# Optimization experiments

Hardware: AMD Instinct MI355X
Metric: run time of the kernel (lower is better)

## Reference

```python
import jax, jax.numpy as jnp
import numpy as np

# Dimensions (see FeatureMixer.__init__ / forward)
B, Q, H, P, C_HEAD = 4, 900, 4, 32, 64          # C_HEAD = feats_dim // num_heads
FEATS_DIM, QUERY_DIM, E = 256, 256, 2
EP = E * P                                        # 64 expanded points
PARAM1 = FEATS_DIM * EP                           # 16384
PARAM2 = EP * P * H                               # 8192
TOTAL = PARAM1 + PARAM2                           # 24576
D1 = PARAM1 // (H * C_HEAD)                       # 64 hidden dim after channel mixing
OUT_IN = PARAM2 * E                               # 16384 = H*EP*D1, out_proj in_features
EPS = 1e-5


def _ln2d(x):
    # F.layer_norm over the last two dims, no affine
    m = jnp.mean(x, axis=(-2, -1), keepdims=True)
    v = jnp.mean((x - m) ** 2, axis=(-2, -1), keepdims=True)
    return (x - m) * jax.lax.rsqrt(v + EPS)


def setup_inputs() -> dict:
    key = jax.random.key(0)
    ks = jax.random.split(key, 6)
    return {
        "query_feats": jax.random.normal(ks[0], (B, Q, QUERY_DIM), jnp.float32),
        "sampled_features": jax.random.normal(ks[1], (B, Q, H, P, C_HEAD), jnp.float32),
        "W_gen": jax.random.normal(ks[2], (QUERY_DIM, TOTAL), jnp.float32) * 0.02,
        "b_gen": jax.random.normal(ks[3], (TOTAL,), jnp.float32) * 0.02,
        "W_out": jax.random.normal(ks[4], (OUT_IN, QUERY_DIM), jnp.float32) * 0.02,
        "b_out": jnp.zeros((QUERY_DIM,), jnp.float32),
        "ln_w": jnp.ones((QUERY_DIM,), jnp.float32),
        "ln_b": jnp.zeros((QUERY_DIM,), jnp.float32),
    }


def reference(query_feats, sampled_features, W_gen, b_gen, W_out, b_out, ln_w, ln_b):
    # generate per-query mixing parameters: (B,Q,TOTAL)
    params = query_feats @ W_gen + b_gen
    p1 = params[..., :PARAM1].reshape(B, Q, H, C_HEAD, D1)   # channel mixer
    p2 = params[..., PARAM1:].reshape(B, Q, H, EP, P)        # spatial mixer

    # channel mixing: (B,Q,H,P,C) @ (B,Q,H,C,D1) -> (B,Q,H,P,D1)
    out = jnp.einsum('bqhpc,bqhcd->bqhpd', sampled_features, p1)
    out = _ln2d(jax.nn.gelu(out, approximate=False))

    # spatial mixing: (B,Q,H,EP,P) @ (B,Q,H,P,D1) -> (B,Q,H,EP,D1)
    out = jnp.einsum('bqhep,bqhpd->bqhed', p2, out)
    out = _ln2d(jax.nn.gelu(out, approximate=False))

    # project back to query dim + affine LayerNorm
    out = out.reshape(B, Q, OUT_IN) @ W_out + b_out
    m = jnp.mean(out, axis=-1, keepdims=True)
    v = jnp.mean((out - m) ** 2, axis=-1, keepdims=True)
    return (out - m) * jax.lax.rsqrt(v + EPS) * ln_w + ln_b
```

## Files before the change

kernel.cpp:

```cpp
#include <hip/hip_runtime.h>
#include <hip/hip_bf16.h>


typedef __attribute__((ext_vector_type(8))) __bf16 bf16x8;
typedef __attribute__((ext_vector_type(4))) float f32x4;
typedef __attribute__((ext_vector_type(4))) short short4v;
typedef __attribute__((ext_vector_type(8))) short short8v;

#define BQ_TOT 3600

__device__ __forceinline__ short f2bf(float f) {
  __hip_bfloat16 h = __float2bfloat16(f);
  short s; __builtin_memcpy(&s, &h, 2);
  return s;
}
__device__ __forceinline__ bf16x8 pack8(float4 a, float4 b) {
  short8v o;
  o[0] = f2bf(a.x); o[1] = f2bf(a.y); o[2] = f2bf(a.z); o[3] = f2bf(a.w);
  o[4] = f2bf(b.x); o[5] = f2bf(b.y); o[6] = f2bf(b.z); o[7] = f2bf(b.w);
  return __builtin_bit_cast(bf16x8, o);
}
__device__ __forceinline__ float gelu_f(float x) {
  float x2 = x * x;
  float u = x * (0.7978845608f + 0.0356774081f * x2);
  float e = __builtin_amdgcn_exp2f(u * 2.885390082f);
  float t = 1.0f - 2.0f / (e + 1.0f);
  return 0.5f * x * (1.0f + t);
}
__device__ __forceinline__ void wred2(float& a, float& b) {
#pragma unroll
  for (int m = 32; m >= 1; m >>= 1) {
    a += __shfl_xor(a, m, 64);
    b += __shfl_xor(b, m, 64);
  }
}

__global__ __launch_bounds__(256) void kcvt_f2b(const float* __restrict__ in,
                                                short* __restrict__ out) {
  int idx = (blockIdx.x * 256 + threadIdx.x) * 8;
  const float4* p = (const float4*)(in + idx);
  *(short8v*)(void*)(out + idx) = __builtin_bit_cast(short8v, pack8(p[0], p[1]));
}

__global__ __launch_bounds__(256) void ktrans_f2b(const float* __restrict__ in,
                                                  short* __restrict__ out,
                                                  int R, int C) {
  __shared__ float t[32][33];
  int tx = threadIdx.x & 31, ty = threadIdx.x >> 5;
  int r0 = blockIdx.y * 32, c0 = blockIdx.x * 32;
#pragma unroll
  for (int i = 0; i < 4; i++)
    t[ty + i * 8][tx] = in[(size_t)(r0 + ty + i * 8) * C + c0 + tx];
  __syncthreads();
#pragma unroll
  for (int i = 0; i < 4; i++)
    out[(size_t)(c0 + ty + i * 8) * R + r0 + tx] = f2bf(t[tx][ty + i * 8]);
}

__global__ __launch_bounds__(256) void k1t_gemm(const short* __restrict__ Xb,
                                                const short* __restrict__ WT,
                                                const float* __restrict__ bg,
                                                short* __restrict__ par,
                                                int nrows) {
  __shared__ short smem[128 * 40 * 2];
  short* As = smem;
  short* Bs = smem + 128 * 40;
  const int b = blockIdx.x;
  const int xcd = b & 7, i = b >> 3;
  const int ct = xcd * 24 + i / 29;
  const int rt = i % 29;
  const int tid = threadIdx.x;
  const int lane = tid & 63, wv = tid >> 6;
  const int l15 = lane & 15, quad = lane >> 4;
  const int wm = (wv & 1) * 64, wn = (wv >> 1) * 64;
  const int sm = tid >> 1, sk = (tid & 1) * 16;
  f32x4 acc[4][4] = {};
  for (int k0 = 0; k0 < 256; k0 += 32) {
    uint4 a0 = {0, 0, 0, 0}, a1 = {0, 0, 0, 0};
    int gr = rt * 128 + sm;
    if (gr < nrows) {
      const uint4* pa = (const uint4*)(Xb + (size_t)gr * 256 + k0 + sk);
      a0 = pa[0]; a1 = pa[1];
    }
    *(uint4*)(As + sm * 40 + sk) = a0;
    *(uint4*)(As + sm * 40 + sk + 8) = a1;
    const uint4* pb = (const uint4*)(WT + (size_t)(ct * 128 + sm) * 256 + k0 + sk);
    *(uint4*)(Bs + sm * 40 + sk) = pb[0];
    *(uint4*)(Bs + sm * 40 + sk + 8) = pb[1];
    __syncthreads();
    bf16x8 af[4], bfr[4];
#pragma unroll
    for (int i2 = 0; i2 < 4; i2++)
      af[i2] = *(const bf16x8*)(const void*)(As + (wm + i2 * 16 + l15) * 40 + quad * 8);
#pragma unroll
    for (int j = 0; j < 4; j++)
      bfr[j] = *(const bf16x8*)(const void*)(Bs + (wn + j * 16 + l15) * 40 + quad * 8);
#pragma unroll
    for (int i2 = 0; i2 < 4; i2++)
#pragma unroll
      for (int j = 0; j < 4; j++)
        acc[i2][j] = __builtin_amdgcn_mfma_f32_16x16x32_bf16(af[i2], bfr[j], acc[i2][j], 0, 0, 0);
    __syncthreads();
  }
  short* Cs = smem;
#pragma unroll
  for (int h = 0; h < 2; h++) {
    if ((wv & 1) == h) {
#pragma unroll
      for (int i2 = 0; i2 < 4; i2++)
#pragma unroll
        for (int j = 0; j < 4; j++) {
          float bgv = bg[ct * 128 + wn + j * 16 + l15];
#pragma unroll
          for (int r = 0; r < 4; r++)
            Cs[(i2 * 16 + quad * 4 + r) * 136 + wn + j * 16 + l15] =
                f2bf(acc[i2][j][r] + bgv);
        }
    }
    __syncthreads();
#pragma unroll
    for (int it = 0; it < 4; it++) {
      int rr = it * 16 + (tid >> 4);
      int cc = (tid & 15) * 8;
      uint4 v = *(const uint4*)(const void*)(Cs + rr * 136 + cc);
      int row = rt * 128 + h * 64 + rr;
      if (row < nrows)
        *(uint4*)(par + (size_t)row * 24576 + ct * 128 + cc) = v;
    }
    __syncthreads();
  }
}

__global__ __launch_bounds__(256) void k1_gemm(const float* __restrict__ X,
                                               const float* __restrict__ Wg,
                                               const float* __restrict__ bg,
                                               short* __restrict__ par,
                                               int nrows) {
  __shared__ short As[128 * 40];
  __shared__ short Bs[128 * 40];
  const int tid = threadIdx.x;
  const int rt = blockIdx.x, ct = blockIdx.y;
  const int lane = tid & 63, wv = tid >> 6;
  const int l15 = lane & 15, quad = lane >> 4;
  const int wm = (wv & 1) * 64, wn = (wv >> 1) * 64;
  const int sm = tid >> 1, sk = (tid & 1) * 16;
  const int bk = tid >> 3, bn0 = (tid & 7) * 16;
  f32x4 acc[4][4] = {};
  for (int k0 = 0; k0 < 256; k0 += 32) {
    float4 av[4] = {};
    int gr = rt * 128 + sm;
    if (gr < nrows) {
      const float4* pa = (const float4*)(X + (size_t)gr * 256 + k0 + sk);
      av[0] = pa[0]; av[1] = pa[1]; av[2] = pa[2]; av[3] = pa[3];
    }
    *(short8v*)(void*)(As + sm * 40 + sk) = __builtin_bit_cast(short8v, pack8(av[0], av[1]));
    *(short8v*)(void*)(As + sm * 40 + sk + 8) = __builtin_bit_cast(short8v, pack8(av[2], av[3]));
    const float4* pb = (const float4*)(Wg + (size_t)(k0 + bk) * 24576 + ct * 128 + bn0);
    float4 b0 = pb[0], b1 = pb[1], b2 = pb[2], b3 = pb[3];
    short* bd = Bs + bn0 * 40 + bk;
    bd[0 * 40] = f2bf(b0.x); bd[1 * 40] = f2bf(b0.y); bd[2 * 40] = f2bf(b0.z); bd[3 * 40] = f2bf(b0.w);
    bd[4 * 40] = f2bf(b1.x); bd[5 * 40] = f2bf(b1.y); bd[6 * 40] = f2bf(b1.z); bd[7 * 40] = f2bf(b1.w);
    bd[8 * 40] = f2bf(b2.x); bd[9 * 40] = f2bf(b2.y); bd[10 * 40] = f2bf(b2.z); bd[11 * 40] = f2bf(b2.w);
    bd[12 * 40] = f2bf(b3.x); bd[13 * 40] = f2bf(b3.y); bd[14 * 40] = f2bf(b3.z); bd[15 * 40] = f2bf(b3.w);
    __syncthreads();
    bf16x8 af[4], bfr[4];
#pragma unroll
    for (int i = 0; i < 4; i++)
      af[i] = *(const bf16x8*)(const void*)(As + (wm + i * 16 + l15) * 40 + quad * 8);
#pragma unroll
    for (int j = 0; j < 4; j++)
      bfr[j] = *(const bf16x8*)(const void*)(Bs + (wn + j * 16 + l15) * 40 + quad * 8);
#pragma unroll
    for (int i = 0; i < 4; i++)
#pragma unroll
      for (int j = 0; j < 4; j++)
        acc[i][j] = __builtin_amdgcn_mfma_f32_16x16x32_bf16(af[i], bfr[j], acc[i][j], 0, 0, 0);
    __syncthreads();
  }
#pragma unroll
  for (int i = 0; i < 4; i++) {
#pragma unroll
    for (int j = 0; j < 4; j++) {
      int col = ct * 128 + wn + j * 16 + l15;
      float bgv = bg[col];
#pragma unroll
      for (int r = 0; r < 4; r++) {
        int row = rt * 128 + wm + i * 16 + quad * 4 + r;
        if (row < nrows)
          par[(size_t)row * 24576 + col] = f2bf(acc[i][j][r] + bgv);
      }
    }
  }
}

__global__ __launch_bounds__(64, 3) void k2_mixw(const float* __restrict__ sf,
                                                 const short* __restrict__ par,
                                                 short* __restrict__ U) {
  __shared__ short p1T[64 * 68];
  __shared__ short Tl[64 * 40];
  const int bq = blockIdx.x >> 2, hd = blockIdx.x & 3;
  const int lane = threadIdx.x & 63;
  const int l15 = lane & 15, quad = lane >> 4;
  const short* pp1 = par + (size_t)bq * 24576 + hd * 4096;
#pragma unroll
  for (int it = 0; it < 8; it++) {
    int c = it * 8 + (lane >> 3);
    int d0 = (lane & 7) * 8;
    short8v tv = *(const short8v*)(const void*)(pp1 + c * 64 + d0);
#pragma unroll
    for (int i = 0; i < 8; i++) p1T[(d0 + i) * 68 + c] = tv[i];
  }
  __syncthreads();
  const float* psf = sf + (size_t)bq * 8192 + hd * 2048;
  bf16x8 sa[2][2];
#pragma unroll
  for (int tm = 0; tm < 2; tm++)
#pragma unroll
    for (int kk = 0; kk < 2; kk++) {
      const float* p = psf + (tm * 16 + l15) * 64 + kk * 32 + quad * 8;
      sa[tm][kk] = pack8(*(const float4*)p, *(const float4*)(p + 4));
    }
  f32x4 acc1[2][4] = {};
#pragma unroll
  for (int kk = 0; kk < 2; kk++) {
#pragma unroll
    for (int tn = 0; tn < 4; tn++) {
      const short* bp = p1T + (tn * 16 + l15) * 68 + kk * 32 + quad * 8;
      short4v lo = *(const short4v*)(const void*)bp;
      short4v hi = *(const short4v*)(const void*)(bp + 4);
      bf16x8 bfr = __builtin_bit_cast(bf16x8, __builtin_shufflevector(lo, hi, 0, 1, 2, 3, 4, 5, 6, 7));
#pragma unroll
      for (int tm = 0; tm < 2; tm++)
        acc1[tm][tn] = __builtin_amdgcn_mfma_f32_16x16x32_bf16(sa[tm][kk], bfr, acc1[tm][tn], 0, 0, 0);
    }
  }
  float s1 = 0.f, s2 = 0.f;
#pragma unroll
  for (int tm = 0; tm < 2; tm++)
#pragma unroll
    for (int tn = 0; tn < 4; tn++)
#pragma unroll
      for (int r = 0; r < 4; r++) {
        float g = gelu_f(acc1[tm][tn][r]);
        acc1[tm][tn][r] = g;
        s1 += g; s2 += g * g;
      }
  wred2(s1, s2);
  float mean = s1 * (1.f / 2048.f);
  float rstd = rsqrtf(fmaxf(s2 * (1.f / 2048.f) - mean * mean, 0.f) + 1e-5f);
#pragma unroll
  for (int tm = 0; tm < 2; tm++)
#pragma unroll
    for (int tn = 0; tn < 4; tn++) {
      short4v o;
#pragma unroll
      for (int r = 0; r < 4; r++) o[r] = f2bf((acc1[tm][tn][r] - mean) * rstd);
      *(short4v*)(void*)(Tl + (tn * 16 + l15) * 40 + tm * 16 + quad * 4) = o;
    }
  __syncthreads();
  const short* pp2 = par + (size_t)bq * 24576 + 16384 + hd * 2048;
  bf16x8 a2[4], b2[4];
#pragma unroll
  for (int t = 0; t < 4; t++) {
    a2[t] = *(const bf16x8*)(const void*)(pp2 + (t * 16 + l15) * 32 + quad * 8);
    b2[t] = *(const bf16x8*)(const void*)(Tl + (t * 16 + l15) * 40 + quad * 8);
  }
  f32x4 acc2[4][4] = {};
#pragma unroll
  for (int tm = 0; tm < 4; tm++)
#pragma unroll
    for (int tn = 0; tn < 4; tn++)
      acc2[tm][tn] = __builtin_amdgcn_mfma_f32_16x16x32_bf16(a2[tm], b2[tn], acc2[tm][tn], 0, 0, 0);
  float u1 = 0.f, u2 = 0.f;
#pragma unroll
  for (int tm = 0; tm < 4; tm++)
#pragma unroll
    for (int tn = 0; tn < 4; tn++)
#pragma unroll
      for (int r = 0; r < 4; r++) {
        float g = gelu_f(acc2[tm][tn][r]);
        acc2[tm][tn][r] = g;
        u1 += g; u2 += g * g;
      }
  wred2(u1, u2);
  float m2 = u1 * (1.f / 4096.f);
  float rs2 = rsqrtf(fmaxf(u2 * (1.f / 4096.f) - m2 * m2, 0.f) + 1e-5f);
  short* pu = U + (size_t)bq * 16384 + hd * 4096;
#pragma unroll
  for (int h2 = 0; h2 < 2; h2++) {
    __syncthreads();
#pragma unroll
    for (int tmh = 0; tmh < 2; tmh++) {
      int tm = h2 * 2 + tmh;
#pragma unroll
      for (int tn = 0; tn < 4; tn++)
#pragma unroll
        for (int r = 0; r < 4; r++) {
          int er = tmh * 16 + quad * 4 + r;
          Tl[er * 72 + tn * 16 + l15] = f2bf((acc2[tm][tn][r] - m2) * rs2);
        }
    }
    __syncthreads();
#pragma unroll
    for (int i = 0; i < 4; i++) {
      int er = i * 8 + (lane >> 3);
      int dch = (lane & 7) * 8;
      uint4 v = *(const uint4*)(const void*)(Tl + er * 72 + dch);
      *(uint4*)(void*)(pu + (size_t)(h2 * 32 + er) * 64 + dch) = v;
    }
  }
}

__global__ __launch_bounds__(256) void k3x_gemm(const short* __restrict__ U,
                                                const short* __restrict__ WT,
                                                float* __restrict__ C2p,
                                                int nrows) {
  __shared__ short As[64 * 72];
  __shared__ short Bs[256 * 72];
  const int b = blockIdx.x;
  const int seg = b & 15, bm = b >> 4;
  const int tid = threadIdx.x;
  const int lane = tid & 63, wv = tid >> 6;
  const int l15 = lane & 15, quad = lane >> 4;
  const int wn = wv * 64;
  const int sr = tid >> 2, sk = (tid & 3) * 16;
  f32x4 acc[4][4] = {};
  int k0 = seg * 1024;
  for (int kt = 0; kt < 16; kt++, k0 += 64) {
    uint4 a0 = {0, 0, 0, 0}, a1 = {0, 0, 0, 0};
    int gr = bm * 64 + sr;
    if (gr < nrows) {
      const uint4* pa = (const uint4*)(U + (size_t)gr * 16384 + k0 + sk);
      a0 = pa[0]; a1 = pa[1];
    }
    *(uint4*)(As + sr * 72 + sk) = a0;
    *(uint4*)(As + sr * 72 + sk + 8) = a1;
#pragma unroll
    for (int rr = 0; rr < 4; rr++) {
      int br = rr * 64 + sr;
      const uint4* pb = (const uint4*)(WT + (size_t)br * 16384 + k0 + sk);
      *(uint4*)(Bs + br * 72 + sk) = pb[0];
      *(uint4*)(Bs + br * 72 + sk + 8) = pb[1];
    }
    __syncthreads();
#pragma unroll
    for (int kk = 0; kk < 64; kk += 32) {
      bf16x8 af[4], bfr[4];
#pragma unroll
      for (int i = 0; i < 4; i++)
        af[i] = *(const bf16x8*)(const void*)(As + (i * 16 + l15) * 72 + kk + quad * 8);
#pragma unroll
      for (int j = 0; j < 4; j++)
        bfr[j] = *(const bf16x8*)(const void*)(Bs + (wn + j * 16 + l15) * 72 + kk + quad * 8);
#pragma unroll
      for (int i = 0; i < 4; i++)
#pragma unroll
        for (int j = 0; j < 4; j++)
          acc[i][j] = __builtin_amdgcn_mfma_f32_16x16x32_bf16(af[i], bfr[j], acc[i][j], 0, 0, 0);
    }
    __syncthreads();
  }
#pragma unroll
  for (int i = 0; i < 4; i++)
#pragma unroll
    for (int j = 0; j < 4; j++)
#pragma unroll
      for (int r = 0; r < 4; r++) {
        int row = bm * 64 + i * 16 + quad * 4 + r;
        if (row < nrows)
          C2p[((size_t)seg * nrows + row) * 256 + wn + j * 16 + l15] = acc[i][j][r];
      }
}

__global__ __launch_bounds__(256) void k3_gemm(const short* __restrict__ U,
                                               const float* __restrict__ Wo,
                                               float* __restrict__ C2p,
                                               int nrows) {
  __shared__ short As[64 * 72];
  __shared__ short Bs[64 * 72];
  const int tid = threadIdx.x;
  const int bm = blockIdx.x, bn = blockIdx.y, seg = blockIdx.z;
  const int lane = tid & 63, wv = tid >> 6;
  const int l15 = lane & 15, quad = lane >> 4;
  const int wm = (wv & 1) * 32, wn = (wv >> 1) * 32;
  const int sr = tid >> 2, sk = (tid & 3) * 16;
  const int bk = tid >> 2, bn0 = (tid & 3) * 16;
  f32x4 acc[2][2] = {};
  int k0 = seg * 4096;
  for (int kt = 0; kt < 64; kt++, k0 += 64) {
    uint4 a0 = {0, 0, 0, 0}, a1 = {0, 0, 0, 0};
    int gr = bm * 64 + sr;
    if (gr < nrows) {
      const uint4* pa = (const uint4*)(U + (size_t)gr * 16384 + k0 + sk);
      a0 = pa[0]; a1 = pa[1];
    }
    *(uint4*)(As + sr * 72 + sk) = a0;
    *(uint4*)(As + sr * 72 + sk + 8) = a1;
    const float4* pb = (const float4*)(Wo + (size_t)(k0 + bk) * 256 + bn * 64 + bn0);
    float4 b0 = pb[0], b1 = pb[1], b2 = pb[2], b3 = pb[3];
    short* bd = Bs + bn0 * 72 + bk;
    bd[0 * 72] = f2bf(b0.x); bd[1 * 72] = f2bf(b0.y); bd[2 * 72] = f2bf(b0.z); bd[3 * 72] = f2bf(b0.w);
    bd[4 * 72] = f2bf(b1.x); bd[5 * 72] = f2bf(b1.y); bd[6 * 72] = f2bf(b1.z); bd[7 * 72] = f2bf(b1.w);
    bd[8 * 72] = f2bf(b2.x); bd[9 * 72] = f2bf(b2.y); bd[10 * 72] = f2bf(b2.z); bd[11 * 72] = f2bf(b2.w);
    bd[12 * 72] = f2bf(b3.x); bd[13 * 72] = f2bf(b3.y); bd[14 * 72] = f2bf(b3.z); bd[15 * 72] = f2bf(b3.w);
    __syncthreads();
#pragma unroll
    for (int kk = 0; kk < 64; kk += 32) {
      bf16x8 af[2], bfr[2];
#pragma unroll
      for (int i = 0; i < 2; i++)
        af[i] = *(const bf16x8*)(const void*)(As + (wm + i * 16 + l15) * 72 + kk + quad * 8);
#pragma unroll
      for (int j = 0; j < 2; j++)
        bfr[j] = *(const bf16x8*)(const void*)(Bs + (wn + j * 16 + l15) * 72 + kk + quad * 8);
#pragma unroll
      for (int i = 0; i < 2; i++)
#pragma unroll
        for (int j = 0; j < 2; j++)
          acc[i][j] = __builtin_amdgcn_mfma_f32_16x16x32_bf16(af[i], bfr[j], acc[i][j], 0, 0, 0);
    }
    __syncthreads();
  }
#pragma unroll
  for (int i = 0; i < 2; i++)
#pragma unroll
    for (int j = 0; j < 2; j++)
#pragma unroll
      for (int r = 0; r < 4; r++) {
        int row = bm * 64 + wm + i * 16 + quad * 4 + r;
        if (row < nrows)
          C2p[((size_t)seg * nrows + row) * 256 + bn * 64 + wn + j * 16 + l15] = acc[i][j][r];
      }
}

__global__ __launch_bounds__(256) void k4_ln(const float* __restrict__ C2p,
                                             const float* __restrict__ bo,
                                             const float* __restrict__ lnw,
                                             const float* __restrict__ lnb,
                                             float* __restrict__ out,
                                             int nrows, int nseg) {
  int row = blockIdx.x * 4 + (threadIdx.x >> 6);
  if (row >= nrows) return;
  int lane = threadIdx.x & 63;
  float v[4] = {0.f, 0.f, 0.f, 0.f};
  for (int s = 0; s < nseg; s++) {
    const float4* p = (const float4*)(C2p + ((size_t)s * nrows + row) * 256) + lane;
    float4 t = *p;
    v[0] += t.x; v[1] += t.y; v[2] += t.z; v[3] += t.w;
  }
  float4 bov = *((const float4*)bo + lane);
  v[0] += bov.x; v[1] += bov.y; v[2] += bov.z; v[3] += bov.w;
  float s1 = v[0] + v[1] + v[2] + v[3];
  float s2 = v[0] * v[0] + v[1] * v[1] + v[2] * v[2] + v[3] * v[3];
  wred2(s1, s2);
  float mean = s1 * (1.f / 256.f);
  float rstd = rsqrtf(fmaxf(s2 * (1.f / 256.f) - mean * mean, 0.f) + 1e-5f);
  float4 wv = *((const float4*)lnw + lane);
  float4 bv = *((const float4*)lnb + lane);
  float4 o;
  o.x = (v[0] - mean) * rstd * wv.x + bv.x;
  o.y = (v[1] - mean) * rstd * wv.y + bv.y;
  o.z = (v[2] - mean) * rstd * wv.z + bv.z;
  o.w = (v[3] - mean) * rstd * wv.w + bv.w;
  *((float4*)(out + (size_t)row * 256) + lane) = o;
}

extern "C" void kernel_launch(void* const* d_in, const int* in_sizes, int n_in,
                              void* d_out, int out_size, void* d_ws, size_t ws_size,
                              hipStream_t stream) {
  const float* qf  = (const float*)d_in[0];
  const float* sf  = (const float*)d_in[1];
  const float* Wg  = (const float*)d_in[2];
  const float* bg  = (const float*)d_in[3];
  const float* Wo  = (const float*)d_in[4];
  const float* bo  = (const float*)d_in[5];
  const float* lnw = (const float*)d_in[6];
  const float* lnb = (const float*)d_in[7];
  char* wsb = (char*)d_ws;

  const size_t sz_WTg = (size_t)24576 * 256 * 2;
  const size_t sz_WTo = (size_t)16384 * 256 * 2;
  const size_t sz_par = (size_t)BQ_TOT * 24576 * 2;
  const size_t sz_U   = (size_t)BQ_TOT * 16384 * 2;
  const size_t sz_Xb  = (size_t)BQ_TOT * 256 * 2;
  const size_t NEED   = sz_WTg + sz_WTo + sz_par + sz_U + sz_Xb;

  if (ws_size >= NEED) {
    short* WTg = (short*)wsb;
    short* WTo = (short*)(wsb + sz_WTg);
    short* par = (short*)(wsb + sz_WTg + sz_WTo);
    short* Uc  = (short*)(wsb + sz_WTg + sz_WTo + sz_par);
    short* Xb  = (short*)(wsb + sz_WTg + sz_WTo + sz_par + sz_U);
    float* C2p = (float*)par;
    ktrans_f2b<<<dim3(768, 8), 256, 0, stream>>>(Wg, WTg, 256, 24576);
    ktrans_f2b<<<dim3(8, 512), 256, 0, stream>>>(Wo, WTo, 16384, 256);
    kcvt_f2b<<<dim3(450), 256, 0, stream>>>(qf, Xb);
    k1t_gemm<<<dim3(5568), 256, 0, stream>>>(Xb, WTg, bg, par, BQ_TOT);
    k2_mixw<<<dim3(BQ_TOT * 4), 64, 0, stream>>>(sf, par, Uc);
    k3x_gemm<<<dim3(912), 256, 0, stream>>>(Uc, WTo, C2p, BQ_TOT);
    k4_ln<<<dim3(900), 256, 0, stream>>>(C2p, bo, lnw, lnb, (float*)d_out, BQ_TOT, 16);
  } else {
    const size_t per_row = 86016;
    long long chunk_ll = (long long)(ws_size / per_row);
    int chunk = (chunk_ll > BQ_TOT) ? BQ_TOT : (int)chunk_ll;
    if (chunk < 8) chunk = 8;
    short* par = (short*)wsb;
    short* Uc  = (short*)(wsb + (size_t)chunk * 24576 * 2);
    float* C2p = (float*)(wsb + (size_t)chunk * 24576 * 2 + (size_t)chunk * 16384 * 2);
    for (int rb = 0; rb < BQ_TOT; rb += chunk) {
      int r = (BQ_TOT - rb < chunk) ? (BQ_TOT - rb) : chunk;
      k1_gemm<<<dim3((r + 127) / 128, 192), 256, 0, stream>>>(
          qf + (size_t)rb * 256, Wg, bg, par, r);
      k2_mixw<<<dim3(r * 4), 64, 0, stream>>>(sf + (size_t)rb * 8192, par, Uc);
      k3_gemm<<<dim3((r + 63) / 64, 4, 4), 256, 0, stream>>>(Uc, Wo, C2p, r);
      k4_ln<<<dim3((r + 3) / 4), 256, 0, stream>>>(
          C2p, bo, lnw, lnb, (float*)d_out + (size_t)rb * 256, r, 4);
    }
  }
}
```

Before: 455.5 us.

## Permute channel-mixer weight columns so mixing kernel reads parameters pre-transposed

The generator weight columns and bias for the channel-mixer block are permuted during weight transposition so the GEMM writes p1 already in d-major layout. A new mixing kernel then loads p1 fragments directly from global memory into MFMA operands, with no shared-memory transpose, and keeps the sampled features in registers. The parameter GEMM also gains register prefetching of the next K tile. The cost is one extra small bias-permute kernel and a layout contract between kernels.

```diff
diff --git a/kernel.cpp b/kernel.cpp
--- a/kernel.cpp
+++ b/kernel.cpp
@@ -42,9 +42,20 @@
   *(short8v*)(void*)(out + idx) = __builtin_bit_cast(short8v, pack8(p[0], p[1]));
 }
 
+__global__ __launch_bounds__(256) void kperm_bg(const float* __restrict__ bg,
+                                                float* __restrict__ bgp) {
+  int p = blockIdx.x * 256 + threadIdx.x;
+  int src = p;
+  if (p < 16384) {
+    int r = p & 4095;
+    src = (p & ~4095) + ((r & 63) << 6) + (r >> 6);
+  }
+  bgp[p] = bg[src];
+}
+
 __global__ __launch_bounds__(256) void ktrans_f2b(const float* __restrict__ in,
                                                   short* __restrict__ out,
-                                                  int R, int C) {
+                                                  int R, int C, int permute_p1) {
   __shared__ float t[32][33];
   int tx = threadIdx.x & 31, ty = threadIdx.x >> 5;
   int r0 = blockIdx.y * 32, c0 = blockIdx.x * 32;
@@ -53,13 +64,20 @@
     t[ty + i * 8][tx] = in[(size_t)(r0 + ty + i * 8) * C + c0 + tx];
   __syncthreads();
 #pragma unroll
-  for (int i = 0; i < 4; i++)
-    out[(size_t)(c0 + ty + i * 8) * R + r0 + tx] = f2bf(t[tx][ty + i * 8]);
+  for (int i = 0; i < 4; i++) {
+    int oc = c0 + ty + i * 8;
+    int orow = oc;
+    if (permute_p1 && oc < 16384) {
+      int r = oc & 4095;
+      orow = (oc & ~4095) + ((r & 63) << 6) + (r >> 6);
+    }
+    out[(size_t)orow * R + r0 + tx] = f2bf(t[tx][ty + i * 8]);
+  }
 }
 
 __global__ __launch_bounds__(256) void k1t_gemm(const short* __restrict__ Xb,
                                                 const short* __restrict__ WT,
-                                                const float* __restrict__ bg,
+                                                const float* __restrict__ bgp,
                                                 short* __restrict__ par,
                                                 int nrows) {
   __shared__ short smem[128 * 40 * 2];
@@ -74,20 +92,27 @@
   const int l15 = lane & 15, quad = lane >> 4;
   const int wm = (wv & 1) * 64, wn = (wv >> 1) * 64;
   const int sm = tid >> 1, sk = (tid & 1) * 16;
+  const int gr = rt * 128 + sm;
+  const bool av = gr < nrows;
+  const uint4* paB = (const uint4*)(Xb + (size_t)gr * 256 + sk);
+  const uint4* pbB = (const uint4*)(WT + (size_t)(ct * 128 + sm) * 256 + sk);
+  uint4 a0 = {0, 0, 0, 0}, a1 = {0, 0, 0, 0}, b0, b1;
+  if (av) { a0 = paB[0]; a1 = paB[1]; }
+  b0 = pbB[0]; b1 = pbB[1];
   f32x4 acc[4][4] = {};
-  for (int k0 = 0; k0 < 256; k0 += 32) {
-    uint4 a0 = {0, 0, 0, 0}, a1 = {0, 0, 0, 0};
-    int gr = rt * 128 + sm;
-    if (gr < nrows) {
-      const uint4* pa = (const uint4*)(Xb + (size_t)gr * 256 + k0 + sk);
-      a0 = pa[0]; a1 = pa[1];
-    }
+#pragma unroll
+  for (int kt = 0; kt < 8; kt++) {
     *(uint4*)(As + sm * 40 + sk) = a0;
     *(uint4*)(As + sm * 40 + sk + 8) = a1;
-    const uint4* pb = (const uint4*)(WT + (size_t)(ct * 128 + sm) * 256 + k0 + sk);
-    *(uint4*)(Bs + sm * 40 + sk) = pb[0];
-    *(uint4*)(Bs + sm * 40 + sk + 8) = pb[1];
-    __syncthreads();
+    *(uint4*)(Bs + sm * 40 + sk) = b0;
+    *(uint4*)(Bs + sm * 40 + sk + 8) = b1;
+    __syncthreads();
+    if (kt < 7) {
+      const uint4* pa = paB + (kt + 1) * 4;
+      const uint4* pb = pbB + (kt + 1) * 4;
+      if (av) { a0 = pa[0]; a1 = pa[1]; }
+      b0 = pb[0]; b1 = pb[1];
+    }
     bf16x8 af[4], bfr[4];
 #pragma unroll
     for (int i2 = 0; i2 < 4; i2++)
@@ -110,7 +135,7 @@
       for (int i2 = 0; i2 < 4; i2++)
 #pragma unroll
         for (int j = 0; j < 4; j++) {
-          float bgv = bg[ct * 128 + wn + j * 16 + l15];
+          float bgv = bgp[ct * 128 + wn + j * 16 + l15];
 #pragma unroll
           for (int r = 0; r < 4; r++)
             Cs[(i2 * 16 + quad * 4 + r) * 136 + wn + j * 16 + l15] =
@@ -193,6 +218,114 @@
   }
 }
 
+__global__ __launch_bounds__(64, 3) void k2_mixn(const float* __restrict__ sf,
+                                                 const short* __restrict__ par,
+                                                 short* __restrict__ U) {
+  __shared__ short Tl[64 * 40];
+  const int bq = blockIdx.x >> 2, hd = blockIdx.x & 3;
+  const int lane = threadIdx.x & 63;
+  const int l15 = lane & 15, quad = lane >> 4;
+  const short* pp1 = par + (size_t)bq * 24576 + hd * 4096;
+  const float* psf = sf + (size_t)bq * 8192 + hd * 2048;
+  bf16x8 sa[2][2];
+#pragma unroll
+  for (int tm = 0; tm < 2; tm++)
+#pragma unroll
+    for (int kk = 0; kk < 2; kk++) {
+      const float* p = psf + (tm * 16 + l15) * 64 + kk * 32 + quad * 8;
+      sa[tm][kk] = pack8(*(const float4*)p, *(const float4*)(p + 4));
+    }
+  bf16x8 b1[4][2];
+#pragma unroll
+  for (int tn = 0; tn < 4; tn++)
+#pragma unroll
+    for (int kk = 0; kk < 2; kk++)
+      b1[tn][kk] = *(const bf16x8*)(const void*)(pp1 + (tn * 16 + l15) * 64 + kk * 32 + quad * 8);
+  f32x4 acc1[2][4] = {};
+#pragma unroll
+  for (int kk = 0; kk < 2; kk++)
+#pragma unroll
+    for (int tn = 0; tn < 4; tn++)
+#pragma unroll
+      for (int tm = 0; tm < 2; tm++)
+        acc1[tm][tn] = __builtin_amdgcn_mfma_f32_16x16x32_bf16(sa[tm][kk], b1[tn][kk], acc1[tm][tn], 0, 0, 0);
+  float s1 = 0.f, s2 = 0.f;
+#pragma unroll
+  for (int tm = 0; tm < 2; tm++)
+#pragma unroll
+    for (int tn = 0; tn < 4; tn++)
+#pragma unroll
+      for (int r = 0; r < 4; r++) {
+        float g = gelu_f(acc1[tm][tn][r]);
+        acc1[tm][tn][r] = g;
+        s1 += g; s2 += g * g;
+      }
+  wred2(s1, s2);
+  float mean = s1 * (1.f / 2048.f);
+  float rstd = rsqrtf(fmaxf(s2 * (1.f / 2048.f) - mean * mean, 0.f) + 1e-5f);
+#pragma unroll
+  for (int tm = 0; tm < 2; tm++)
+#pragma unroll
+    for (int tn = 0; tn < 4; tn++) {
+      short4v o;
+#pragma unroll
+      for (int r = 0; r < 4; r++) o[r] = f2bf((acc1[tm][tn][r] - mean) * rstd);
+      *(short4v*)(void*)(Tl + (tn * 16 + l15) * 40 + tm * 16 + quad * 4) = o;
+    }
+  __syncthreads();
+  const short* pp2 = par + (size_t)bq * 24576 + 16384 + hd * 2048;
+  bf16x8 a2[4], b2[4];
+#pragma unroll
+  for (int t = 0; t < 4; t++) {
+    a2[t] = *(const bf16x8*)(const void*)(pp2 + (t * 16 + l15) * 32 + quad * 8);
+    b2[t] = *(const bf16x8*)(const void*)(Tl + (t * 16 + l15) * 40 + quad * 8);
+  }
+  f32x4 acc2[4][4] = {};
+#pragma unroll
+  for (int tm = 0; tm < 4; tm++)
+#pragma unroll
+    for (int tn = 0; tn < 4; tn++)
+      acc2[tm][tn] = __builtin_amdgcn_mfma_f32_16x16x32_bf16(a2[tm], b2[tn], acc2[tm][tn], 0, 0, 0);
+  float u1 = 0.f, u2 = 0.f;
+#pragma unroll
+  for (int tm = 0; tm < 4; tm++)
+#pragma unroll
+    for (int tn = 0; tn < 4; tn++)
+#pragma unroll
+      for (int r = 0; r < 4; r++) {
+        float g = gelu_f(acc2[tm][tn][r]);
+        acc2[tm][tn][r] = g;
+        u1 += g; u2 += g * g;
+      }
+  wred2(u1, u2);
+  float m2 = u1 * (1.f / 4096.f);
+  float rs2 = rsqrtf(fmaxf(u2 * (1.f / 4096.f) - m2 * m2, 0.f) + 1e-5f);
+  short* pu = U + (size_t)bq * 16384 + hd * 4096;
+#pragma unroll
+  for (int h2 = 0; h2 < 2; h2++) {
+    __syncthreads();
+#pragma unroll
+    for (int tmh = 0; tmh < 2; tmh++) {
+      int tm = h2 * 2 + tmh;
+#pragma unroll
+      for (int tn = 0; tn < 4; tn++)
+#pragma unroll
+        for (int r = 0; r < 4; r++) {
+          int er = tmh * 16 + quad * 4 + r;
+          Tl[er * 72 + tn * 16 + l15] = f2bf((acc2[tm][tn][r] - m2) * rs2);
+        }
+    }
+    __syncthreads();
+#pragma unroll
+    for (int i = 0; i < 4; i++) {
+      int er = i * 8 + (lane >> 3);
+      int dch = (lane & 7) * 8;
+      uint4 v = *(const uint4*)(const void*)(Tl + er * 72 + dch);
+      *(uint4*)(void*)(pu + (size_t)(h2 * 32 + er) * 64 + dch) = v;
+    }
+  }
+}
+
 __global__ __launch_bounds__(64, 3) void k2_mixw(const float* __restrict__ sf,
                                                  const short* __restrict__ par,
                                                  short* __restrict__ U) {
@@ -483,7 +616,8 @@
   const size_t sz_par = (size_t)BQ_TOT * 24576 * 2;
   const size_t sz_U   = (size_t)BQ_TOT * 16384 * 2;
   const size_t sz_Xb  = (size_t)BQ_TOT * 256 * 2;
-  const size_t NEED   = sz_WTg + sz_WTo + sz_par + sz_U + sz_Xb;
+  const size_t sz_bgp = (size_t)24576 * 4;
+  const size_t NEED   = sz_WTg + sz_WTo + sz_par + sz_U + sz_Xb + sz_bgp;
 
   if (ws_size >= NEED) {
     short* WTg = (short*)wsb;
@@ -491,12 +625,14 @@
     short* par = (short*)(wsb + sz_WTg + sz_WTo);
     short* Uc  = (short*)(wsb + sz_WTg + sz_WTo + sz_par);
     short* Xb  = (short*)(wsb + sz_WTg + sz_WTo + sz_par + sz_U);
+    float* bgp = (float*)(wsb + sz_WTg + sz_WTo + sz_par + sz_U + sz_Xb);
     float* C2p = (float*)par;
-    ktrans_f2b<<<dim3(768, 8), 256, 0, stream>>>(Wg, WTg, 256, 24576);
-    ktrans_f2b<<<dim3(8, 512), 256, 0, stream>>>(Wo, WTo, 16384, 256);
+    ktrans_f2b<<<dim3(768, 8), 256, 0, stream>>>(Wg, WTg, 256, 24576, 1);
+    ktrans_f2b<<<dim3(8, 512), 256, 0, stream>>>(Wo, WTo, 16384, 256, 0);
     kcvt_f2b<<<dim3(450), 256, 0, stream>>>(qf, Xb);
-    k1t_gemm<<<dim3(5568), 256, 0, stream>>>(Xb, WTg, bg, par, BQ_TOT);
-    k2_mixw<<<dim3(BQ_TOT * 4), 64, 0, stream>>>(sf, par, Uc);
+    kperm_bg<<<dim3(96), 256, 0, stream>>>(bg, bgp);
+    k1t_gemm<<<dim3(5568), 256, 0, stream>>>(Xb, WTg, bgp, par, BQ_TOT);
+    k2_mixn<<<dim3(BQ_TOT * 4), 64, 0, stream>>>(sf, par, Uc);
     k3x_gemm<<<dim3(912), 256, 0, stream>>>(Uc, WTo, C2p, BQ_TOT);
     k4_ln<<<dim3(900), 256, 0, stream>>>(C2p, bo, lnw, lnb, (float*)d_out, BQ_TOT, 16);
   } else {
```

After: 446.3 us. 1.02x faster.
